# Kernel tuning notes

Hardware: AMD Instinct MI355X
Metric: run time of the kernel (lower is better)

## Reference

```python
import jax, jax.numpy as jnp
import numpy as np

B, H, L = 8, 256, 8192

def setup_inputs() -> dict:
    key = jax.random.key(0)
    k1, k2, k3 = jax.random.split(key, 3)
    u = jax.random.normal(k1, (B, H, L), dtype=jnp.float32)
    K = jax.random.normal(k2, (H, L), dtype=jnp.float32)
    # D ~ uniform_ring with min=max=1.0, field='real' -> random signs on unit ring
    D = jnp.where(jax.random.uniform(k3, (H,)) < 0.5, -1.0, 1.0).astype(jnp.float32)
    return {"u": u, "K": K, "D": D}

def reference(u, K, D):
    # FFT-based circular long convolution per channel: y = ifft(fft(u) * fft(K)).real
    u_s = jnp.fft.fft(u, axis=-1)            # (B,H,L) complex
    k_s = jnp.fft.fft(K, axis=-1)            # (H,L)   complex
    y = jnp.fft.ifft(u_s * k_s[None], axis=-1).real  # (B,H,L)
    y = y + D[None, :, None] * u             # skip connection D*u
    y = jnp.tanh(y)
    return y
```

## Files before the change

kernel.cpp:

```cpp
#include <hip/hip_runtime.h>
#include <math.h>


#define LL 8192
#define NT 256
#define HH 256
#define TWO_PI 6.2831853071795864f
#define CP16 0.980785280403230f
#define SP16 0.195090322016128f
#define CP8  0.92387953251129f
#define SP8  0.38268343236509f

__device__ __forceinline__ int SW(int e) {
    return e ^ ((e >> 4) & 15) ^ (((e >> 8) & 1) << 4);
}
__device__ __forceinline__ float fast_tanh(float x) {
    float e = __expf(2.0f * x);
    return 1.0f - 2.0f / (e + 1.0f);
}

template<int JT>
__device__ __forceinline__ void fill_pyr_cs(float c0, float s0, float Er, float Ei,
                                            float* twr, float* twi) {
    const int off = (1 << JT) - 1;
    twr[off] = c0; twi[off] = s0;
    #pragma unroll
    for (int m = 1; m < (1 << JT); ++m) {
        const float pr = twr[off + m - 1], pi = twi[off + m - 1];
        twr[off + m] = pr * Er - pi * Ei;
        twi[off + m] = pr * Ei + pi * Er;
    }
    #pragma unroll
    for (int j = JT - 1; j >= 0; --j) {
        #pragma unroll
        for (int m = 0; m < (1 << j); ++m) {
            const float a = twr[(2 << j) - 1 + m], b = twi[(2 << j) - 1 + m];
            twr[(1 << j) - 1 + m] = a * a - b * b;
            twi[(1 << j) - 1 + m] = 2.0f * a * b;
        }
    }
}
template<int JT>
__device__ __forceinline__ void fill_pyr(float ang0, float Er, float Ei,
                                         float* twr, float* twi) {
    float s, c;
    __sincosf(ang0, &s, &c);
    fill_pyr_cs<JT>(c, s, Er, Ei, twr, twi);
}

template<int R2>
__device__ __forceinline__ void dif_apply(float* xr, float* xi,
                                          const float* twr, const float* twi) {
    #pragma unroll
    for (int j = R2 - 1; j >= 0; --j) {
        #pragma unroll
        for (int q = 0; q < (1 << (R2 - 1)); ++q) {
            const int mm = q & ((1 << j) - 1);
            const int m0 = ((q >> j) << (j + 1)) | mm;
            const int m1 = m0 + (1 << j);
            const float wr = twr[(1 << j) - 1 + mm], wi = twi[(1 << j) - 1 + mm];
            const float ar = xr[m0], ai = xi[m0], br = xr[m1], bi = xi[m1];
            xr[m0] = ar + br; xi[m0] = ai + bi;
            const float dr = ar - br, di = ai - bi;
            xr[m1] = dr * wr - di * wi;
            xi[m1] = dr * wi + di * wr;
        }
    }
}
template<int R2>
__device__ __forceinline__ void dit_apply(float* xr, float* xi,
                                          const float* twr, const float* twi) {
    #pragma unroll
    for (int j = 0; j < R2; ++j) {
        #pragma unroll
        for (int q = 0; q < (1 << (R2 - 1)); ++q) {
            const int mm = q & ((1 << j) - 1);
            const int m0 = ((q >> j) << (j + 1)) | mm;
            const int m1 = m0 + (1 << j);
            const float wr = twr[(1 << j) - 1 + mm], wi = twi[(1 << j) - 1 + mm];
            const float br = xr[m1] * wr - xi[m1] * wi;
            const float bi = xr[m1] * wi + xi[m1] * wr;
            const float ar = xr[m0], ai = xi[m0];
            xr[m0] = ar + br; xi[m0] = ai + bi;
            xr[m1] = ar - br; xi[m1] = ai - bi;
        }
    }
}

__device__ __forceinline__ void fwd_A(float* xr, float* xi, int tid,
                                      float* re, float* im) {
    float twr[31], twi[31];
    fill_pyr<4>(-(TWO_PI / 8192.0f) * (float)tid, CP16, -SP16, twr, twi);
    dif_apply<5>(xr, xi, twr, twi);
    #pragma unroll
    for (int m = 0; m < 32; ++m) {
        const int p = SW(tid + (m << 8));
        re[p] = xr[m]; im[p] = xi[m];
    }
}

__global__ __launch_bounds__(NT) void kfft_kernel(const float* __restrict__ K,
                                                  const float* __restrict__ D,
                                                  float2* __restrict__ Kf) {
    __shared__ float re[LL];
    __shared__ float im[LL];
    const int h = blockIdx.x;
    const int tid = threadIdx.x;
    const float* Kr = K + (size_t)h * LL;
    float xr[32], xi[32];
    #pragma unroll
    for (int m = 0; m < 32; ++m) {
        xr[m] = Kr[tid + (m << 8)];
        xi[m] = 0.0f;
    }
    fwd_A(xr, xi, tid, re, im);
    __syncthreads();

    const int lane = tid & 63, wv = tid >> 6;
    const int q = lane & 15, qw = (lane >> 4) & 3;

    {
        float twr[15], twi[15];
        fill_pyr<3>(-(TWO_PI / 256.0f) * (float)q, CP8, -SP8, twr, twi);
        #pragma unroll
        for (int r = 0; r < 2; ++r) {
            const int c = (wv << 3) + qw + (r << 2);
            const int base = (c << 8) + q;
            float ar[16], ai[16];
            #pragma unroll
            for (int m = 0; m < 16; ++m) {
                const int p = SW(base + (m << 4));
                ar[m] = re[p]; ai[m] = im[p];
            }
            dif_apply<4>(ar, ai, twr, twi);
            #pragma unroll
            for (int m = 0; m < 16; ++m) {
                const int p = SW(base + (m << 4));
                re[p] = ar[m]; im[p] = ai[m];
            }
        }
    }
    {
        const float dh = D[h];
        const float invN = 1.0f / (float)LL;
        float twr[15], twi[15];
        fill_pyr_cs<3>(1.0f, 0.0f, CP8, -SP8, twr, twi);
        #pragma unroll
        for (int r = 0; r < 2; ++r) {
            const int c = (wv << 3) + qw + (r << 2);
            const int eb = (c << 8) + (q << 4);
            float yr[16], yi[16];
            #pragma unroll
            for (int j = 0; j < 16; ++j) {
                const int p = SW(eb + j);
                yr[j] = re[p]; yi[j] = im[p];
            }
            dif_apply<4>(yr, yi, twr, twi);
            float4* o4 = (float4*)(Kf + (size_t)h * LL + eb);
            #pragma unroll
            for (int jj = 0; jj < 8; ++jj) {
                float4 v;
                v.x = (yr[2 * jj]     + dh) * invN; v.y = yi[2 * jj]     * invN;
                v.z = (yr[2 * jj + 1] + dh) * invN; v.w = yi[2 * jj + 1] * invN;
                o4[jj] = v;
            }
        }
    }
}

__global__ __launch_bounds__(NT) void conv_kernel(const float* __restrict__ u,
                                                  const float2* __restrict__ Kf,
                                                  float* __restrict__ out) {
    __shared__ float re[LL];
    __shared__ float im[LL];
    const int tid = threadIdx.x;
    const int h = blockIdx.x & (HH - 1);
    const int pr_ = blockIdx.x >> 8;
    const size_t off0 = ((size_t)(pr_ * 2) * HH + h) * LL;
    const size_t off1 = off0 + (size_t)HH * LL;
    const float* u0 = u + off0;
    const float* u1 = u + off1;

    float xr[32], xi[32];
    #pragma unroll
    for (int m = 0; m < 32; ++m) {
        xr[m] = u0[tid + (m << 8)];
        xi[m] = u1[tid + (m << 8)];
    }
    fwd_A(xr, xi, tid, re, im);
    __syncthreads();

    const int lane = tid & 63, wv = tid >> 6;
    const int q = lane & 15, qw = (lane >> 4) & 3;
    const int c0 = (wv << 3) + qw;
    const float2* kf = Kf + (size_t)h * LL;

    float kwr[2][16], kwi[2][16];
    #pragma unroll
    for (int r = 0; r < 2; ++r) {
        const int eb = ((c0 + (r << 2)) << 8) + (q << 4);
        const float4* kp = (const float4*)(kf + eb);
        #pragma unroll
        for (int jj = 0; jj < 8; ++jj) {
            const float4 v = kp[jj];
            kwr[r][2 * jj] = v.x;     kwi[r][2 * jj] = v.y;
            kwr[r][2 * jj + 1] = v.z; kwi[r][2 * jj + 1] = v.w;
        }
    }

    {
        float twr[15], twi[15];
        fill_pyr<3>(-(TWO_PI / 256.0f) * (float)q, CP8, -SP8, twr, twi);
        #pragma unroll
        for (int r = 0; r < 2; ++r) {
            const int base = ((c0 + (r << 2)) << 8) + q;
            float ar[16], ai[16];
            #pragma unroll
            for (int m = 0; m < 16; ++m) {
                const int p = SW(base + (m << 4));
                ar[m] = re[p]; ai[m] = im[p];
            }
            dif_apply<4>(ar, ai, twr, twi);
            #pragma unroll
            for (int m = 0; m < 16; ++m) {
                const int p = SW(base + (m << 4));
                re[p] = ar[m]; im[p] = ai[m];
            }
        }
    }
    {
        float twd_r[15], twd_i[15], twu_r[15], twu_i[15];
        fill_pyr_cs<3>(1.0f, 0.0f, CP8, -SP8, twd_r, twd_i);
        fill_pyr_cs<3>(1.0f, 0.0f, CP8, SP8, twu_r, twu_i);
        #pragma unroll
        for (int r = 0; r < 2; ++r) {
            const int eb = ((c0 + (r << 2)) << 8) + (q << 4);
            float yr[16], yi[16];
            #pragma unroll
            for (int j = 0; j < 16; ++j) {
                const int p = SW(eb + j);
                yr[j] = re[p]; yi[j] = im[p];
            }
            dif_apply<4>(yr, yi, twd_r, twd_i);
            #pragma unroll
            for (int j = 0; j < 16; ++j) {
                const float a = yr[j], b = yi[j];
                yr[j] = a * kwr[r][j] - b * kwi[r][j];
                yi[j] = a * kwi[r][j] + b * kwr[r][j];
            }
            dit_apply<4>(yr, yi, twu_r, twu_i);
            #pragma unroll
            for (int j = 0; j < 16; ++j) {
                const int p = SW(eb + j);
                re[p] = yr[j]; im[p] = yi[j];
            }
        }
    }
    {
        float twr[15], twi[15];
        fill_pyr<3>((TWO_PI / 256.0f) * (float)q, CP8, SP8, twr, twi);
        #pragma unroll
        for (int r = 0; r < 2; ++r) {
            const int base = ((c0 + (r << 2)) << 8) + q;
            float ar[16], ai[16];
            #pragma unroll
            for (int m = 0; m < 16; ++m) {
                const int p = SW(base + (m << 4));
                ar[m] = re[p]; ai[m] = im[p];
            }
            dit_apply<4>(ar, ai, twr, twi);
            #pragma unroll
            for (int m = 0; m < 16; ++m) {
                const int p = SW(base + (m << 4));
                re[p] = ar[m]; im[p] = ai[m];
            }
        }
    }
    __syncthreads();

    {
        float twr[31], twi[31];
        #pragma unroll
        for (int m = 0; m < 32; ++m) {
            const int p = SW(tid + (m << 8));
            xr[m] = re[p]; xi[m] = im[p];
        }
        fill_pyr<4>((TWO_PI / 8192.0f) * (float)tid, CP16, SP16, twr, twi);
        dit_apply<5>(xr, xi, twr, twi);
    }
    float* o0 = out + off0;
    float* o1 = out + off1;
    #pragma unroll
    for (int m = 0; m < 32; ++m) {
        const int n = tid + (m << 8);
        o0[n] = fast_tanh(xr[m]);
        o1[n] = fast_tanh(xi[m]);
    }
}

extern "C" void kernel_launch(void* const* d_in, const int* in_sizes, int n_in,
                              void* d_out, int out_size, void* d_ws, size_t ws_size,
                              hipStream_t stream) {
    const float* u = (const float*)d_in[0];
    const float* K = (const float*)d_in[1];
    const float* D = (const float*)d_in[2];
    float* out = (float*)d_out;
    float2* Kf = (float2*)d_ws;

    kfft_kernel<<<dim3(HH), dim3(NT), 0, stream>>>(K, D, Kf);
    conv_kernel<<<dim3(4 * HH), dim3(NT), 0, stream>>>(u, Kf, out);
}
```

Before: 153.2 us.

## Halve conv kernel shared memory by staging real and imaginary parts through one buffer

The conv kernel now uses a single 32 KB shared buffer instead of separate real and imaginary arrays. It transposes real and imaginary parts one after the other, keeping the middle-stage data in registers and doing the inner transposes within each wavefront's own rows. The aim is to cut LDS use per block so more blocks fit per CU. The cost is extra barriers, more LDS round trips, and higher register pressure from holding ar/ai[2][16] plus xr/xi, which could cancel the occupancy gain.

```diff
diff --git a/kernel.cpp b/kernel.cpp
--- a/kernel.cpp
+++ b/kernel.cpp
@@ -87,8 +87,8 @@
     }
 }
 
-__device__ __forceinline__ void fwd_A(float* xr, float* xi, int tid,
-                                      float* re, float* im) {
+__device__ __forceinline__ void fwd_A64(float* xr, float* xi, int tid,
+                                        float* re, float* im) {
     float twr[31], twi[31];
     fill_pyr<4>(-(TWO_PI / 8192.0f) * (float)tid, CP16, -SP16, twr, twi);
     dif_apply<5>(xr, xi, twr, twi);
@@ -113,7 +113,7 @@
         xr[m] = Kr[tid + (m << 8)];
         xi[m] = 0.0f;
     }
-    fwd_A(xr, xi, tid, re, im);
+    fwd_A64(xr, xi, tid, re, im);
     __syncthreads();
 
     const int lane = tid & 63, wv = tid >> 6;
@@ -171,8 +171,7 @@
 __global__ __launch_bounds__(NT) void conv_kernel(const float* __restrict__ u,
                                                   const float2* __restrict__ Kf,
                                                   float* __restrict__ out) {
-    __shared__ float re[LL];
-    __shared__ float im[LL];
+    __shared__ float buf[LL];
     const int tid = threadIdx.x;
     const int h = blockIdx.x & (HH - 1);
     const int pr_ = blockIdx.x >> 8;
@@ -187,104 +186,115 @@
         xr[m] = u0[tid + (m << 8)];
         xi[m] = u1[tid + (m << 8)];
     }
-    fwd_A(xr, xi, tid, re, im);
-    __syncthreads();
-
+    {
+        float twr[31], twi[31];
+        fill_pyr<4>(-(TWO_PI / 8192.0f) * (float)tid, CP16, -SP16, twr, twi);
+        dif_apply<5>(xr, xi, twr, twi);
+    }
     const int lane = tid & 63, wv = tid >> 6;
     const int q = lane & 15, qw = (lane >> 4) & 3;
     const int c0 = (wv << 3) + qw;
+
+    #pragma unroll
+    for (int m = 0; m < 32; ++m) buf[SW(tid + (m << 8))] = xr[m];
+    __syncthreads();
+    float ar[2][16], ai[2][16];
+    #pragma unroll
+    for (int r = 0; r < 2; ++r) {
+        #pragma unroll
+        for (int m = 0; m < 16; ++m)
+            ar[r][m] = buf[SW(((c0 + (r << 2)) << 8) + q + (m << 4))];
+    }
+    __syncthreads();
+    #pragma unroll
+    for (int m = 0; m < 32; ++m) buf[SW(tid + (m << 8))] = xi[m];
+    __syncthreads();
+    #pragma unroll
+    for (int r = 0; r < 2; ++r) {
+        #pragma unroll
+        for (int m = 0; m < 16; ++m)
+            ai[r][m] = buf[SW(((c0 + (r << 2)) << 8) + q + (m << 4))];
+    }
+
     const float2* kf = Kf + (size_t)h * LL;
-
-    float kwr[2][16], kwi[2][16];
-    #pragma unroll
-    for (int r = 0; r < 2; ++r) {
-        const int eb = ((c0 + (r << 2)) << 8) + (q << 4);
-        const float4* kp = (const float4*)(kf + eb);
-        #pragma unroll
-        for (int jj = 0; jj < 8; ++jj) {
-            const float4 v = kp[jj];
-            kwr[r][2 * jj] = v.x;     kwi[r][2 * jj] = v.y;
-            kwr[r][2 * jj + 1] = v.z; kwi[r][2 * jj + 1] = v.w;
-        }
-    }
-
-    {
-        float twr[15], twi[15];
-        fill_pyr<3>(-(TWO_PI / 256.0f) * (float)q, CP8, -SP8, twr, twi);
-        #pragma unroll
-        for (int r = 0; r < 2; ++r) {
-            const int base = ((c0 + (r << 2)) << 8) + q;
-            float ar[16], ai[16];
-            #pragma unroll
-            for (int m = 0; m < 16; ++m) {
-                const int p = SW(base + (m << 4));
-                ar[m] = re[p]; ai[m] = im[p];
-            }
-            dif_apply<4>(ar, ai, twr, twi);
-            #pragma unroll
-            for (int m = 0; m < 16; ++m) {
-                const int p = SW(base + (m << 4));
-                re[p] = ar[m]; im[p] = ai[m];
-            }
-        }
-    }
-    {
-        float twd_r[15], twd_i[15], twu_r[15], twu_i[15];
-        fill_pyr_cs<3>(1.0f, 0.0f, CP8, -SP8, twd_r, twd_i);
-        fill_pyr_cs<3>(1.0f, 0.0f, CP8, SP8, twu_r, twu_i);
-        #pragma unroll
-        for (int r = 0; r < 2; ++r) {
-            const int eb = ((c0 + (r << 2)) << 8) + (q << 4);
-            float yr[16], yi[16];
-            #pragma unroll
-            for (int j = 0; j < 16; ++j) {
-                const int p = SW(eb + j);
-                yr[j] = re[p]; yi[j] = im[p];
-            }
-            dif_apply<4>(yr, yi, twd_r, twd_i);
+    #pragma unroll
+    for (int r = 0; r < 2; ++r) {
+        const int cb = (c0 + (r << 2)) << 8;
+        float kwr[16], kwi[16];
+        {
+            const float4* kp = (const float4*)(kf + cb + (q << 4));
+            #pragma unroll
+            for (int jj = 0; jj < 8; ++jj) {
+                const float4 v = kp[jj];
+                kwr[2 * jj] = v.x;     kwi[2 * jj] = v.y;
+                kwr[2 * jj + 1] = v.z; kwi[2 * jj + 1] = v.w;
+            }
+        }
+        {
+            float t1r[15], t1i[15];
+            fill_pyr<3>(-(TWO_PI / 256.0f) * (float)q, CP8, -SP8, t1r, t1i);
+            dif_apply<4>(ar[r], ai[r], t1r, t1i);
+        }
+        float yr[16], yi[16];
+        #pragma unroll
+        for (int m = 0; m < 16; ++m) buf[SW(cb + q + (m << 4))] = ar[r][m];
+        #pragma unroll
+        for (int j = 0; j < 16; ++j) yr[j] = buf[SW(cb + (q << 4) + j)];
+        #pragma unroll
+        for (int m = 0; m < 16; ++m) buf[SW(cb + q + (m << 4))] = ai[r][m];
+        #pragma unroll
+        for (int j = 0; j < 16; ++j) yi[j] = buf[SW(cb + (q << 4) + j)];
+        {
+            float tdr[15], tdi[15];
+            fill_pyr_cs<3>(1.0f, 0.0f, CP8, -SP8, tdr, tdi);
+            dif_apply<4>(yr, yi, tdr, tdi);
             #pragma unroll
             for (int j = 0; j < 16; ++j) {
                 const float a = yr[j], b = yi[j];
-                yr[j] = a * kwr[r][j] - b * kwi[r][j];
-                yi[j] = a * kwi[r][j] + b * kwr[r][j];
-            }
-            dit_apply<4>(yr, yi, twu_r, twu_i);
-            #pragma unroll
-            for (int j = 0; j < 16; ++j) {
-                const int p = SW(eb + j);
-                re[p] = yr[j]; im[p] = yi[j];
-            }
-        }
-    }
-    {
-        float twr[15], twi[15];
-        fill_pyr<3>((TWO_PI / 256.0f) * (float)q, CP8, SP8, twr, twi);
-        #pragma unroll
-        for (int r = 0; r < 2; ++r) {
-            const int base = ((c0 + (r << 2)) << 8) + q;
-            float ar[16], ai[16];
-            #pragma unroll
-            for (int m = 0; m < 16; ++m) {
-                const int p = SW(base + (m << 4));
-                ar[m] = re[p]; ai[m] = im[p];
-            }
-            dit_apply<4>(ar, ai, twr, twi);
-            #pragma unroll
-            for (int m = 0; m < 16; ++m) {
-                const int p = SW(base + (m << 4));
-                re[p] = ar[m]; im[p] = ai[m];
-            }
-        }
-    }
-    __syncthreads();
+                yr[j] = a * kwr[j] - b * kwi[j];
+                yi[j] = a * kwi[j] + b * kwr[j];
+            }
+            float tur[15], tui[15];
+            fill_pyr_cs<3>(1.0f, 0.0f, CP8, SP8, tur, tui);
+            dit_apply<4>(yr, yi, tur, tui);
+        }
+        #pragma unroll
+        for (int j = 0; j < 16; ++j) buf[SW(cb + (q << 4) + j)] = yr[j];
+        #pragma unroll
+        for (int m = 0; m < 16; ++m) ar[r][m] = buf[SW(cb + q + (m << 4))];
+        #pragma unroll
+        for (int j = 0; j < 16; ++j) buf[SW(cb + (q << 4) + j)] = yi[j];
+        #pragma unroll
+        for (int m = 0; m < 16; ++m) ai[r][m] = buf[SW(cb + q + (m << 4))];
+        {
+            float t1r[15], t1i[15];
+            fill_pyr<3>((TWO_PI / 256.0f) * (float)q, CP8, SP8, t1r, t1i);
+            dit_apply<4>(ar[r], ai[r], t1r, t1i);
+        }
+    }
+
+    #pragma unroll
+    for (int r = 0; r < 2; ++r) {
+        #pragma unroll
+        for (int m = 0; m < 16; ++m)
+            buf[SW(((c0 + (r << 2)) << 8) + q + (m << 4))] = ar[r][m];
+    }
+    __syncthreads();
+    #pragma unroll
+    for (int m = 0; m < 32; ++m) xr[m] = buf[SW(tid + (m << 8))];
+    __syncthreads();
+    #pragma unroll
+    for (int r = 0; r < 2; ++r) {
+        #pragma unroll
+        for (int m = 0; m < 16; ++m)
+            buf[SW(((c0 + (r << 2)) << 8) + q + (m << 4))] = ai[r][m];
+    }
+    __syncthreads();
+    #pragma unroll
+    for (int m = 0; m < 32; ++m) xi[m] = buf[SW(tid + (m << 8))];
 
     {
         float twr[31], twi[31];
-        #pragma unroll
-        for (int m = 0; m < 32; ++m) {
-            const int p = SW(tid + (m << 8));
-            xr[m] = re[p]; xi[m] = im[p];
-        }
         fill_pyr<4>((TWO_PI / 8192.0f) * (float)tid, CP16, SP16, twr, twi);
         dit_apply<5>(xr, xi, twr, twi);
     }
```

New measurement: 190.8 us. 24.6% more time.
